# Performance work log

Measured on AMD Instinct MI355X. Metric: run time of the kernel, lower is better.

The kernel has to match this reference:

```python
import jax, jax.numpy as jnp
import numpy as np

N, R, B, H, C, E = 4096, 8, 30, 64, 16, 131072


def setup_inputs() -> dict:
    key = jax.random.key(0)
    ks = jax.random.split(key, 11)
    s = 0.02  # small init scale for weights
    return {
        "x": jax.random.normal(ks[0], (N, N), jnp.float32),
        "edge_index": jax.random.randint(ks[1], (2, E), 0, N, jnp.int32),
        "edge_type": jax.random.randint(ks[2], (E,), 0, R, jnp.int32),
        "basis1": jax.random.normal(ks[3], (B, N, H), jnp.float32) * s,
        "att1": jax.random.normal(ks[4], (R, B), jnp.float32) * s,
        "root1": jax.random.normal(ks[5], (N, H), jnp.float32) * s,
        "bias1": jnp.zeros((H,), jnp.float32),
        "basis2": jax.random.normal(ks[6], (B, H, C), jnp.float32) * s,
        "att2": jax.random.normal(ks[7], (R, B), jnp.float32) * s,
        "root2": jax.random.normal(ks[8], (H, C), jnp.float32) * s,
        "bias2": jnp.zeros((C,), jnp.float32),
    }


def _rgcn_conv(x, src, dst, etype, deg_inv, basis, att, root, bias):
    # Basis-decomposed relation weights: W_r = sum_b att[r,b] * basis[b]
    W = jnp.einsum("rb,bio->rio", att, basis)            # [R, in, out]
    # Pre-transform every node by every relation weight (equivalent to
    # per-edge bmm(x_j, W[edge_type]) but avoids gathering [E, in] features).
    h = jnp.einsum("ni,rio->nro", x, W)                  # [N, R, out]
    msg = h[src, etype]                                  # [E, out] per-edge message
    agg = jax.ops.segment_sum(msg, dst, num_segments=N)  # scatter-add to dst
    agg = agg * deg_inv[:, None]                         # scatter-mean (aggr='mean')
    return agg + x @ root + bias                         # root/self transform + bias


def reference(x, edge_index, edge_type, basis1, att1, root1, bias1,
              basis2, att2, root2, bias2):
    src, dst = edge_index[0], edge_index[1]
    deg = jax.ops.segment_sum(jnp.ones((E,), jnp.float32), dst, num_segments=N)
    deg_inv = 1.0 / jnp.maximum(deg, 1.0)  # zero in-degree -> 0 output, as scatter_mean
    h = jax.nn.relu(_rgcn_conv(x, src, dst, edge_type, deg_inv,
                               basis1, att1, root1, bias1))
    out = _rgcn_conv(h, src, dst, edge_type, deg_inv,
                     basis2, att2, root2, bias2)
    return jax.nn.log_softmax(out, axis=1)
```

## Files before the change

### kernel.cpp

```cpp
#include <hip/hip_runtime.h>
#include <cstdint>

#define E_CNT 131072
#define N_CNT 4096

typedef short bf16x8 __attribute__((ext_vector_type(8)));
typedef float f32x4 __attribute__((ext_vector_type(4)));

__device__ __forceinline__ ushort f2bf(float f) {
  union { float f; unsigned u; } v; v.f = f;
  unsigned r = v.u + 0x7FFFu + ((v.u >> 16) & 1u);
  return (ushort)(r >> 16);
}

__global__ __launch_bounds__(256) void k_zero_deg(int* __restrict__ p) {
  p[blockIdx.x * 256 + threadIdx.x] = 0;
}

__global__ __launch_bounds__(256) void k_prep(const float4* __restrict__ x,
                                              ushort* __restrict__ xbf,
                                              const int* __restrict__ dstp,
                                              int* __restrict__ deg,
                                              const float* __restrict__ att1,
                                              const float* __restrict__ basis1,
                                              float* __restrict__ wtmp,
                                              int* __restrict__ c1i) {
  int bid = blockIdx.x, tid = threadIdx.x;
  if (bid < 16384) {
    int i = bid * 256 + tid;
    float4 v = x[i];
    ushort4 o;
    o.x = f2bf(v.x); o.y = f2bf(v.y); o.z = f2bf(v.z); o.w = f2bf(v.w);
    *(ushort4*)(xbf + (size_t)i * 4) = o;
  } else if (bid < 16896) {
    int e = (bid - 16384) * 256 + tid;
    atomicAdd(&deg[dstp[e]], 1);
  } else if (bid < 17920) {
    int flat = (bid - 16896) * 256 + tid;
    float a[8] = {0.f, 0.f, 0.f, 0.f, 0.f, 0.f, 0.f, 0.f};
    for (int b = 0; b < 30; ++b) {
      float v = basis1[(size_t)b * 262144 + flat];
#pragma unroll
      for (int r = 0; r < 8; ++r) a[r] += att1[r * 30 + b] * v;
    }
#pragma unroll
    for (int r = 0; r < 8; ++r) wtmp[(size_t)r * 262144 + flat] = a[r];
  } else {
    int flat = (bid - 17920) * 256 + tid;
    c1i[flat] = 0;
  }
}

__global__ __launch_bounds__(1024) void k_scan(const int* __restrict__ deg,
                                               int* __restrict__ rowptr,
                                               int* __restrict__ cursor,
                                               float* __restrict__ dinv) {
  __shared__ int part[1024];
  int t = threadIdx.x;
  int base = t * 4;
  int d0 = deg[base], d1 = deg[base + 1], d2 = deg[base + 2], d3 = deg[base + 3];
  int s = d0 + d1 + d2 + d3;
  part[t] = s;
  __syncthreads();
  for (int off = 1; off < 1024; off <<= 1) {
    int v = part[t];
    int u = (t >= off) ? part[t - off] : 0;
    __syncthreads();
    part[t] = v + u;
    __syncthreads();
  }
  int incl = part[t];
  int excl = incl - s;
  int p0 = excl, p1 = excl + d0, p2 = p1 + d1, p3 = p2 + d2;
  rowptr[base] = p0; rowptr[base + 1] = p1; rowptr[base + 2] = p2; rowptr[base + 3] = p3;
  cursor[base] = p0; cursor[base + 1] = p1; cursor[base + 2] = p2; cursor[base + 3] = p3;
  dinv[base]     = 1.0f / fmaxf((float)d0, 1.0f);
  dinv[base + 1] = 1.0f / fmaxf((float)d1, 1.0f);
  dinv[base + 2] = 1.0f / fmaxf((float)d2, 1.0f);
  dinv[base + 3] = 1.0f / fmaxf((float)d3, 1.0f);
  if (t == 1023) rowptr[4096] = incl;
}

__global__ __launch_bounds__(256) void k_mid(const int* __restrict__ srcp,
                                             const int* __restrict__ dstp,
                                             const int* __restrict__ et,
                                             int* __restrict__ cursor,
                                             int* __restrict__ spack,
                                             const float* __restrict__ wtmp,
                                             const float* __restrict__ root1,
                                             ushort* __restrict__ wt1,
                                             const float* __restrict__ att2,
                                             const float* __restrict__ basis2,
                                             const float* __restrict__ root2,
                                             float* __restrict__ w2e) {
  __shared__ float tile[64 * 65];
  int bid = blockIdx.x, t = threadIdx.x;
  if (bid < 512) {
    int e = bid * 256 + t;
    int d = dstp[e];
    int pos = atomicAdd(&cursor[d], 1);
    spack[pos] = (srcp[e] << 3) | et[e];
  } else if (bid < 1088) {
    int bb = bid - 512;
    int r = bb >> 6;
    int i0 = (bb & 63) * 64;
    const float* sp = (r < 8) ? (wtmp + (size_t)r * 262144) : root1;
#pragma unroll
    for (int it = 0; it < 16; ++it) {
      int flat = it * 256 + t;
      int il = flat >> 6, o = flat & 63;
      tile[il * 65 + o] = sp[(size_t)(i0 + il) * 64 + o];
    }
    __syncthreads();
#pragma unroll
    for (int it = 0; it < 16; ++it) {
      int flat = it * 256 + t;
      int o = flat >> 6, il = flat & 63;
      wt1[(size_t)(r * 64 + o) * 4096 + i0 + il] = f2bf(tile[il * 65 + o]);
    }
  } else {
    int r = bid - 1088;
    for (int q = t; q < 1024; q += 256) {
      float a = 0.f;
      if (r < 8) {
        for (int b = 0; b < 30; ++b) a += att2[r * 30 + b] * basis2[b * 1024 + q];
      } else {
        a = root2[q];
      }
      w2e[r * 1024 + q] = a;
    }
  }
}

#define SPLITK 4
#define KSTEPS 16
__global__ __launch_bounds__(256) void k_gemm1(const ushort* __restrict__ xbf,
                                               const ushort* __restrict__ wt1,
                                               float* __restrict__ c1) {
  __shared__ __align__(16) ushort As[2][128 * 64];
  __shared__ __align__(16) ushort Bs[2][64 * 64];
  int bid = blockIdx.x;
  int swz = (bid & 7) * 144 + (bid >> 3);
  int kp = swz / 288, t2 = swz % 288;
  int bm = t2 / 9, bn = t2 % 9;
  int m0 = bm * 128, n0 = bn * 64, kbase = kp * 1024;
  int tid = threadIdx.x;
  int lane = tid & 63, wid = tid >> 6;
  int wm = wid >> 1, wn = wid & 1;

  f32x4 acc[4][2] = {};

  auto stage = [&](int buf, int k0) {
#pragma unroll
    for (int it = 0; it < 4; ++it) {
      int flat = it * 256 + tid;
      int row = flat >> 3, gg = flat & 7;
      int gcol = k0 + ((gg ^ (row & 7)) << 3);
      const ushort* g = xbf + (size_t)(m0 + row) * 4096 + gcol;
      ushort* l = &As[buf][(it * 256 + wid * 64) * 8];
      __builtin_amdgcn_global_load_lds((const __attribute__((address_space(1))) void*)g,
                                       (__attribute__((address_space(3))) void*)l, 16, 0, 0);
    }
#pragma unroll
    for (int it = 0; it < 2; ++it) {
      int flat = it * 256 + tid;
      int row = flat >> 3, gg = flat & 7;
      int gcol = k0 + ((gg ^ (row & 7)) << 3);
      const ushort* g = wt1 + (size_t)(n0 + row) * 4096 + gcol;
      ushort* l = &Bs[buf][(it * 256 + wid * 64) * 8];
      __builtin_amdgcn_global_load_lds((const __attribute__((address_space(1))) void*)g,
                                       (__attribute__((address_space(3))) void*)l, 16, 0, 0);
    }
  };

  stage(0, kbase);
  __syncthreads();
  int cur = 0;
  for (int t = 0; t < KSTEPS; ++t) {
    if (t + 1 < KSTEPS) stage(cur ^ 1, kbase + (t + 1) * 64);
#pragma unroll
    for (int ks = 0; ks < 2; ++ks) {
      int q = lane >> 4, sw = lane & 7;
      bf16x8 bfr[2];
#pragma unroll
      for (int ni = 0; ni < 2; ++ni) {
        int row = wn * 32 + ni * 16 + (lane & 15);
        bfr[ni] = *(const bf16x8*)&Bs[cur][row * 64 + (((ks * 4 + q) ^ sw) << 3)];
      }
#pragma unroll
      for (int mi = 0; mi < 4; ++mi) {
        int row = wm * 64 + mi * 16 + (lane & 15);
        bf16x8 afr = *(const bf16x8*)&As[cur][row * 64 + (((ks * 4 + q) ^ sw) << 3)];
#pragma unroll
        for (int ni = 0; ni < 2; ++ni)
          acc[mi][ni] = __builtin_amdgcn_mfma_f32_16x16x32_bf16(afr, bfr[ni], acc[mi][ni], 0, 0, 0);
      }
    }
    __syncthreads();
    cur ^= 1;
  }

  int cf = lane & 15, rf4 = (lane >> 4) * 4;
#pragma unroll
  for (int mi = 0; mi < 4; ++mi)
#pragma unroll
    for (int ni = 0; ni < 2; ++ni) {
      int gcol = n0 + wn * 32 + ni * 16 + cf;
#pragma unroll
      for (int j = 0; j < 4; ++j) {
        int grow = m0 + wm * 64 + mi * 16 + rf4 + j;
        atomicAdd(&c1[(size_t)grow * 576 + gcol], acc[mi][ni][j]);
      }
    }
}

__global__ __launch_bounds__(64) void k_agg1h2(const float* __restrict__ c1,
                                               const int* __restrict__ rowptr,
                                               const int* __restrict__ spack,
                                               const float* __restrict__ dinv,
                                               const float* __restrict__ bias1,
                                               const float* __restrict__ w2e,
                                               float* __restrict__ h2c) {
  __shared__ float sh[64];
  int n = blockIdx.x, t = threadIdx.x;
  int s0 = rowptr[n], s1 = rowptr[n + 1];
  float acc = 0.f;
  for (int e = s0; e < s1; ++e) {
    int p = spack[e];
    acc += c1[(size_t)(p >> 3) * 576 + (p & 7) * 64 + t];
  }
  float v = acc * dinv[n] + c1[(size_t)n * 576 + 512 + t] + bias1[t];
  sh[t] = fmaxf(v, 0.f);
  __syncthreads();
  float* o = h2c + (size_t)n * 144;
  for (int rc = t; rc < 144; rc += 64) {
    int r9 = rc >> 4, c = rc & 15;
    const float* w = w2e + r9 * 1024 + c;
    float a = 0.f;
#pragma unroll
    for (int hh = 0; hh < 64; ++hh) a += sh[hh] * w[hh * 16];
    o[rc] = a;
  }
}

__global__ __launch_bounds__(64) void k_agg2(const float* __restrict__ h2c,
                                             const int* __restrict__ rowptr,
                                             const int* __restrict__ spack,
                                             const float* __restrict__ dinv,
                                             const float* __restrict__ bias2,
                                             float* __restrict__ out) {
  __shared__ float red[64];
  int n = blockIdx.x, t = threadIdx.x;
  int c = t & 15, q = t >> 4;
  int s0 = rowptr[n], s1 = rowptr[n + 1];
  float acc = 0.f;
  for (int e = s0 + q; e < s1; e += 4) {
    int p = spack[e];
    acc += h2c[(size_t)(p >> 3) * 144 + (p & 7) * 16 + c];
  }
  red[t] = acc;
  __syncthreads();
  if (t < 16) {
    float sum = red[c] + red[16 + c] + red[32 + c] + red[48 + c];
    float v = sum * dinv[n] + h2c[(size_t)n * 144 + 128 + c] + bias2[c];
    float m = v;
#pragma unroll
    for (int off = 1; off < 16; off <<= 1) m = fmaxf(m, __shfl_xor(m, off, 64));
    float ex = expf(v - m);
    float s = ex;
#pragma unroll
    for (int off = 1; off < 16; off <<= 1) s += __shfl_xor(s, off, 64);
    out[n * 16 + c] = v - m - logf(s);
  }
}

extern "C" void kernel_launch(void* const* d_in, const int* in_sizes, int n_in,
                              void* d_out, int out_size, void* d_ws, size_t ws_size,
                              hipStream_t stream) {
  const float* x      = (const float*)d_in[0];
  const int*   ei     = (const int*)d_in[1];
  const int*   et     = (const int*)d_in[2];
  const float* basis1 = (const float*)d_in[3];
  const float* att1   = (const float*)d_in[4];
  const float* root1  = (const float*)d_in[5];
  const float* bias1  = (const float*)d_in[6];
  const float* basis2 = (const float*)d_in[7];
  const float* att2   = (const float*)d_in[8];
  const float* root2  = (const float*)d_in[9];
  const float* bias2  = (const float*)d_in[10];
  float* out = (float*)d_out;

  char* ws = (char*)d_ws;
  size_t off = 0;
  auto alloc = [&](size_t bytes) {
    void* p = ws + off;
    off = (off + bytes + 255) & ~(size_t)255;
    return p;
  };
  ushort* xbf  = (ushort*)alloc((size_t)N_CNT * N_CNT * 2);
  ushort* wt1  = (ushort*)alloc((size_t)576 * 4096 * 2);
  float*  wtmp = (float*)alloc((size_t)8 * N_CNT * 64 * 4);
  float*  c1   = (float*)alloc((size_t)N_CNT * 576 * 4);
  float*  w2e  = (float*)alloc((size_t)9 * 64 * 16 * 4);
  float*  h2c  = (float*)alloc((size_t)N_CNT * 144 * 4);
  int*    deg    = (int*)alloc(4096 * 4);
  float*  dinv   = (float*)alloc(4096 * 4);
  int*    rowptr = (int*)alloc(4097 * 4);
  int*    cursor = (int*)alloc(4096 * 4);
  int*    spack  = (int*)alloc((size_t)E_CNT * 4);

  const int* srcp = ei;
  const int* dstp = ei + E_CNT;

  k_zero_deg<<<16, 256, 0, stream>>>(deg);
  k_prep<<<27136, 256, 0, stream>>>((const float4*)x, xbf, dstp, deg,
                                    att1, basis1, wtmp, (int*)c1);
  k_scan<<<1, 1024, 0, stream>>>(deg, rowptr, cursor, dinv);
  k_mid<<<1097, 256, 0, stream>>>(srcp, dstp, et, cursor, spack,
                                  wtmp, root1, wt1, att2, basis2, root2, w2e);
  k_gemm1<<<1152, 256, 0, stream>>>(xbf, wt1, c1);
  k_agg1h2<<<4096, 64, 0, stream>>>(c1, rowptr, spack, dinv, bias1, w2e, h2c);
  k_agg2<<<4096, 64, 0, stream>>>(h2c, rowptr, spack, dinv, bias2, out);
}
```

Baseline: 158.3 us.

## Load GEMM fragments directly from global memory and unroll edge aggregation

The split-K GEMM drops its LDS double-buffering and loads each wave's MFMA A/B fragments straight from global memory into registers, removing LDS staging and block-wide barriers. Because the two waves in each row or column of the block share tiles, the same data is fetched more than once through the caches, and each lane reads 16-byte chunks spread across rows, which coalesces poorly. Separately, the per-node edge aggregation loop is unrolled by four so more independent gathers are in flight at once.

```diff
diff --git a/kernel.cpp b/kernel.cpp
--- a/kernel.cpp
+++ b/kernel.cpp
@@ -132,72 +132,43 @@
   }
 }
 
-#define SPLITK 4
-#define KSTEPS 16
 __global__ __launch_bounds__(256) void k_gemm1(const ushort* __restrict__ xbf,
                                                const ushort* __restrict__ wt1,
                                                float* __restrict__ c1) {
-  __shared__ __align__(16) ushort As[2][128 * 64];
-  __shared__ __align__(16) ushort Bs[2][64 * 64];
   int bid = blockIdx.x;
   int swz = (bid & 7) * 144 + (bid >> 3);
   int kp = swz / 288, t2 = swz % 288;
   int bm = t2 / 9, bn = t2 % 9;
   int m0 = bm * 128, n0 = bn * 64, kbase = kp * 1024;
-  int tid = threadIdx.x;
-  int lane = tid & 63, wid = tid >> 6;
+  int lane = threadIdx.x & 63, wid = threadIdx.x >> 6;
   int wm = wid >> 1, wn = wid & 1;
+  int r16 = lane & 15, q8 = (lane >> 4) * 8;
+
+  const ushort* Ab = xbf + (size_t)(m0 + wm * 64 + r16) * 4096 + kbase + q8;
+  const ushort* Bb = wt1 + (size_t)(n0 + wn * 32 + r16) * 4096 + kbase + q8;
 
   f32x4 acc[4][2] = {};
 
-  auto stage = [&](int buf, int k0) {
-#pragma unroll
-    for (int it = 0; it < 4; ++it) {
-      int flat = it * 256 + tid;
-      int row = flat >> 3, gg = flat & 7;
-      int gcol = k0 + ((gg ^ (row & 7)) << 3);
-      const ushort* g = xbf + (size_t)(m0 + row) * 4096 + gcol;
-      ushort* l = &As[buf][(it * 256 + wid * 64) * 8];
-      __builtin_amdgcn_global_load_lds((const __attribute__((address_space(1))) void*)g,
-                                       (__attribute__((address_space(3))) void*)l, 16, 0, 0);
-    }
-#pragma unroll
-    for (int it = 0; it < 2; ++it) {
-      int flat = it * 256 + tid;
-      int row = flat >> 3, gg = flat & 7;
-      int gcol = k0 + ((gg ^ (row & 7)) << 3);
-      const ushort* g = wt1 + (size_t)(n0 + row) * 4096 + gcol;
-      ushort* l = &Bs[buf][(it * 256 + wid * 64) * 8];
-      __builtin_amdgcn_global_load_lds((const __attribute__((address_space(1))) void*)g,
-                                       (__attribute__((address_space(3))) void*)l, 16, 0, 0);
-    }
-  };
-
-  stage(0, kbase);
-  __syncthreads();
-  int cur = 0;
-  for (int t = 0; t < KSTEPS; ++t) {
-    if (t + 1 < KSTEPS) stage(cur ^ 1, kbase + (t + 1) * 64);
+#pragma unroll 4
+  for (int t = 0; t < 16; ++t) {
+    int ko = t * 64;
+    bf16x8 a[2][4], b[2][2];
 #pragma unroll
     for (int ks = 0; ks < 2; ++ks) {
-      int q = lane >> 4, sw = lane & 7;
-      bf16x8 bfr[2];
-#pragma unroll
-      for (int ni = 0; ni < 2; ++ni) {
-        int row = wn * 32 + ni * 16 + (lane & 15);
-        bfr[ni] = *(const bf16x8*)&Bs[cur][row * 64 + (((ks * 4 + q) ^ sw) << 3)];
-      }
-#pragma unroll
-      for (int mi = 0; mi < 4; ++mi) {
-        int row = wm * 64 + mi * 16 + (lane & 15);
-        bf16x8 afr = *(const bf16x8*)&As[cur][row * 64 + (((ks * 4 + q) ^ sw) << 3)];
+#pragma unroll
+      for (int mi = 0; mi < 4; ++mi)
+        a[ks][mi] = *(const bf16x8*)(Ab + (size_t)mi * 16 * 4096 + ko + ks * 32);
+#pragma unroll
+      for (int ni = 0; ni < 2; ++ni)
+        b[ks][ni] = *(const bf16x8*)(Bb + (size_t)ni * 16 * 4096 + ko + ks * 32);
+    }
+#pragma unroll
+    for (int ks = 0; ks < 2; ++ks)
+#pragma unroll
+      for (int mi = 0; mi < 4; ++mi)
 #pragma unroll
         for (int ni = 0; ni < 2; ++ni)
-          acc[mi][ni] = __builtin_amdgcn_mfma_f32_16x16x32_bf16(afr, bfr[ni], acc[mi][ni], 0, 0, 0);
-      }
-    }
-    __syncthreads();
-    cur ^= 1;
+          acc[mi][ni] = __builtin_amdgcn_mfma_f32_16x16x32_bf16(a[ks][mi], b[ks][ni], acc[mi][ni], 0, 0, 0);
   }
 
   int cf = lane & 15, rf4 = (lane >> 4) * 4;
@@ -225,7 +196,16 @@
   int n = blockIdx.x, t = threadIdx.x;
   int s0 = rowptr[n], s1 = rowptr[n + 1];
   float acc = 0.f;
-  for (int e = s0; e < s1; ++e) {
+  int e = s0;
+  for (; e + 3 < s1; e += 4) {
+    int p0 = spack[e], p1 = spack[e + 1], p2 = spack[e + 2], p3 = spack[e + 3];
+    float v0 = c1[(size_t)(p0 >> 3) * 576 + (p0 & 7) * 64 + t];
+    float v1 = c1[(size_t)(p1 >> 3) * 576 + (p1 & 7) * 64 + t];
+    float v2 = c1[(size_t)(p2 >> 3) * 576 + (p2 & 7) * 64 + t];
+    float v3 = c1[(size_t)(p3 >> 3) * 576 + (p3 & 7) * 64 + t];
+    acc += (v0 + v1) + (v2 + v3);
+  }
+  for (; e < s1; ++e) {
     int p = spack[e];
     acc += c1[(size_t)(p >> 3) * 576 + (p & 7) * 64 + t];
   }
```

New measurement: 235.7 us. +48.9%, slower.
